# Kernel optimization log

Hardware: AMD Instinct MI355X
Metric: run time of the kernel (lower is better)

Reference implementation:

```python
import jax, jax.numpy as jnp
import numpy as np

HEADS = 16  # matches init_kwargs


def setup_inputs() -> dict:
    key = jax.random.key(0)
    ks = jax.random.split(key, 9)
    N, L, E, D = 2, 2048, 1024, 64
    return {
        "query": jax.random.normal(ks[0], (N, L, E), dtype=jnp.float32),
        "keys": jax.random.normal(ks[1], (N, L, E), dtype=jnp.float32),
        "values": jax.random.normal(ks[2], (N, L, E), dtype=jnp.float32),
        "masks": jax.random.randint(ks[3], (N, 1, 1, L), 0, 2, dtype=jnp.int32),
        "Wq": jax.random.normal(ks[4], (D, D), dtype=jnp.float32) / np.sqrt(D),
        "Wk": jax.random.normal(ks[5], (D, D), dtype=jnp.float32) / np.sqrt(D),
        "Wv": jax.random.normal(ks[6], (D, D), dtype=jnp.float32) / np.sqrt(D),
        "Wo": jax.random.normal(ks[7], (E, E), dtype=jnp.float32) / np.sqrt(E),
        "bo": jax.random.normal(ks[8], (E,), dtype=jnp.float32),
    }


def reference(query, keys, values, masks, Wq, Wk, Wv, Wo, bo):
    N, Lq, E = query.shape
    Lk = keys.shape[1]
    H = HEADS
    D = E // H
    # split heads: [N, L, H, D]
    q = query.reshape(N, Lq, H, D)
    k = keys.reshape(N, Lk, H, D)
    v = values.reshape(N, Lk, H, D)
    # per-head linear projections (weights shared across heads); Linear: x @ W.T
    q = jnp.einsum("nqhd,ed->nqhe", q, Wq)
    k = jnp.einsum("nkhd,ed->nkhe", k, Wk)
    v = jnp.einsum("nkhd,ed->nkhe", v, Wv)
    # scores [N, H, Lq, Lk]
    scores = jnp.einsum("nqhd,nkhd->nhqk", q, k)
    scores = jnp.where(masks == 0, jnp.float32(-1e20), scores)
    # NOTE: original scales by sqrt(embed_size), not sqrt(head_dim)
    attn = jax.nn.softmax(scores / jnp.sqrt(jnp.float32(E)), axis=3)
    out = jnp.einsum("nhqk,nkhd->nqhd", attn, v).reshape(N, Lq, E)
    return out @ Wo.T + bo
```

## Files before the change

kernel.cpp:

```cpp
#include <hip/hip_runtime.h>


typedef __bf16 bf16_t;
typedef __bf16 bf16x4 __attribute__((ext_vector_type(4)));
typedef __bf16 bf16x8 __attribute__((ext_vector_type(8)));
typedef float f32x4 __attribute__((ext_vector_type(4)));
typedef unsigned int u32x4 __attribute__((ext_vector_type(4)));

#define MFMA16(a, b, c) __builtin_amdgcn_mfma_f32_16x16x32_bf16((a), (b), (c), 0, 0, 0)

#define GLOAD_LDS16(gp, lp)                                              \
    __builtin_amdgcn_global_load_lds(                                    \
        (const __attribute__((address_space(1))) void*)(gp),             \
        (__attribute__((address_space(3))) void*)(lp), 16, 0, 0)

__device__ inline bf16x8 cvt8(const float* __restrict__ p) {
    f32x4 a = *(const f32x4*)p;
    f32x4 b = *(const f32x4*)(p + 4);
    bf16x8 r;
    r[0] = (bf16_t)a[0]; r[1] = (bf16_t)a[1];
    r[2] = (bf16_t)a[2]; r[3] = (bf16_t)a[3];
    r[4] = (bf16_t)b[0]; r[5] = (bf16_t)b[1];
    r[6] = (bf16_t)b[2]; r[7] = (bf16_t)b[3];
    return r;
}

__device__ inline bf16x8 cvt8s(const f32x4 a, const f32x4 b) {
    bf16x8 r;
    r[0] = (bf16_t)a[0]; r[1] = (bf16_t)a[1];
    r[2] = (bf16_t)a[2]; r[3] = (bf16_t)a[3];
    r[4] = (bf16_t)b[0]; r[5] = (bf16_t)b[1];
    r[6] = (bf16_t)b[2]; r[7] = (bf16_t)b[3];
    return r;
}

__device__ inline float exp2_fast(float x) {
    float r;
    asm("v_exp_f32 %0, %1" : "=v"(r) : "v"(x));
    return r;
}

__device__ inline unsigned cvt_pk_bf16(float lo, float hi) {
    unsigned r;
    asm("v_cvt_pk_bf16_f32 %0, %1, %2" : "=v"(r) : "v"(lo), "v"(hi));
    return r;
}

__device__ inline void xchg_quads(unsigned &x, unsigned &y) {
    asm("v_permlane32_swap_b32 %0, %1\n\t"
        "v_permlane16_swap_b32 %0, %1"
        : "+v"(x), "+v"(y));
}

__global__ __launch_bounds__(256) void scan_kernel(
    const int* __restrict__ msk, int* __restrict__ excl, int* __restrict__ lmap,
    const float* __restrict__ Wq, const float* __restrict__ Wk,
    const float* __restrict__ Wv,
    bf16_t* __restrict__ Wqb, bf16_t* __restrict__ Wkb, bf16_t* __restrict__ Wvb)
{
    const int t = threadIdx.x;

    if (blockIdx.x >= 2) {
        const int wi = blockIdx.x - 2;
        const float* Ws = (wi == 0) ? Wq : (wi == 1) ? Wk : Wv;
        bf16_t* Wb = (wi == 0) ? Wqb : (wi == 1) ? Wkb : Wvb;
        const float scale = (wi == 0) ? 0.04508422f : 1.0f;
        #pragma unroll
        for (int j = 0; j < 4; j++) {
            int idx = t * 16 + j * 4;
            f32x4 v = *(const f32x4*)&Ws[idx];
            bf16x4 r;
            r[0] = (bf16_t)(v[0] * scale); r[1] = (bf16_t)(v[1] * scale);
            r[2] = (bf16_t)(v[2] * scale); r[3] = (bf16_t)(v[3] * scale);
            *(bf16x4*)&Wb[idx] = r;
        }
        return;
    }

    __shared__ int wsum[4];
    const int n = blockIdx.x;
    const int lane = t & 63, w = t >> 6;
    const int* m = msk + n * 2048;
    int* e = excl + n * 2049;
    int* lm = lmap + n * 2048;

    int v[8], s = 0;
    #pragma unroll
    for (int j = 0; j < 8; j++) { v[j] = (m[t * 8 + j] != 0); s += v[j]; }

    int inc = s;
    #pragma unroll
    for (int d = 1; d < 64; d <<= 1) {
        int o = __shfl_up(inc, d);
        if (lane >= d) inc += o;
    }
    if (lane == 63) wsum[w] = inc;
    __syncthreads();
    int off = 0;
    #pragma unroll
    for (int i = 0; i < 4; i++)
        if (i < w) off += wsum[i];

    int a = off + inc - s;
    #pragma unroll
    for (int j = 0; j < 8; j++) {
        e[t * 8 + j] = a;
        if (v[j]) lm[a] = t * 8 + j;
        a += v[j];
    }
    if (t == 255) e[2048] = a;
}

__global__ __launch_bounds__(256) void qkv_proj_kernel(
    const float* __restrict__ kin, const float* __restrict__ vin,
    const bf16_t* __restrict__ Wkb, const bf16_t* __restrict__ Wvb,
    const float* __restrict__ Wo,
    const int* __restrict__ excl, const int* __restrict__ lmap,
    bf16_t* __restrict__ kc, bf16_t* __restrict__ vcT, bf16_t* __restrict__ Wob)
{
    __shared__ __align__(16) char smem[51200];

    const int t = threadIdx.x;
    const int w = t >> 6, lane = t & 63, quad = lane >> 4, l16 = lane & 15;

    if (blockIdx.y == 2) {
        int idx = blockIdx.x * 1024 + t * 4;
        f32x4 v = *(const f32x4*)&Wo[idx];
        bf16x4 r;
        r[0] = (bf16_t)v[0]; r[1] = (bf16_t)v[1];
        r[2] = (bf16_t)v[2]; r[3] = (bf16_t)v[3];
        *(bf16x4*)&Wob[idx] = r;
        return;
    }

    if (blockIdx.y == 1) {
        bf16_t* Ct = (bf16_t*)smem;
        const int h = blockIdx.x & 15;
        const int ctile = blockIdx.x >> 4;
        const int n = ctile >> 5;
        const int c0 = (ctile & 31) * 64;
        const int Lc = excl[n * 2049 + 2048];
        if (c0 >= Lc) return;

        const int p0 = w * 16 + l16;
        int cs = c0 + p0; if (cs > Lc - 1) cs = Lc - 1;
        const int tg = lmap[n * 2048 + cs];
        const size_t rb = ((size_t)(n * 2048 + tg)) * 1024 + h * 64;

        bf16x8 b0 = cvt8(&vin[rb + quad * 8]);
        bf16x8 b1 = cvt8(&vin[rb + 32 + quad * 8]);

        #pragma unroll
        for (int nt = 0; nt < 4; nt++) {
            bf16x8 a0 = *(const bf16x8*)&Wvb[(nt * 16 + l16) * 64 + quad * 8];
            bf16x8 a1 = *(const bf16x8*)&Wvb[(nt * 16 + l16) * 64 + 32 + quad * 8];
            f32x4 acc = {0.f, 0.f, 0.f, 0.f};
            acc = MFMA16(a0, b0, acc);
            acc = MFMA16(a1, b1, acc);
            #pragma unroll
            for (int r = 0; r < 4; r++)
                Ct[(nt * 16 + quad * 4 + r) * 72 + w * 16 + l16] = (bf16_t)acc[r];
        }
        __syncthreads();
        const int cnt = (Lc - c0 < 64) ? (Lc - c0) : 64;
        const size_t ob2 = ((size_t)(n * 16 + h)) * 131072 + c0;
        #pragma unroll
        for (int pass = 0; pass < 2; pass++) {
            int r = pass * 32 + (t >> 3);
            int cb8 = (t & 7) * 8;
            if (cb8 < cnt) {
                if (cb8 + 8 <= cnt) {
                    *(bf16x8*)&vcT[ob2 + (size_t)r * 2048 + cb8] =
                        *(const bf16x8*)&Ct[r * 72 + cb8];
                } else {
                    for (int q = cb8; q < cnt; q++)
                        vcT[ob2 + (size_t)r * 2048 + q] = Ct[r * 72 + q];
                }
            }
        }
        return;
    }

    if (blockIdx.x >= 512) return;
    const int n = blockIdx.x >> 8;
    const int c0 = (blockIdx.x & 255) * 8;
    const int Lc = excl[n * 2049 + 2048];
    if (c0 >= Lc) return;

    float* Xs = (float*)smem;
    bf16_t* Ct2 = (bf16_t*)(smem + 32768);

    #pragma unroll
    for (int j = 0; j < 8; j++) {
        int br = w * 32 + j * 4;
        int srow = br + (lane >> 4);
        int scol = ((lane & 15) ^ (srow & 15)) * 4;
        int csx = c0 + (srow >> 4); if (csx > Lc - 1) csx = Lc - 1;
        int hs = srow & 15;
        int ls = lmap[n * 2048 + csx];
        GLOAD_LDS16(&kin[((size_t)((n * 2048 + ls) * 16 + hs)) * 64 + scol], &Xs[br * 64]);
    }
    __syncthreads();

    const int rbase = w * 32;
    bf16x8 a[2][2];
    #pragma unroll
    for (int qs = 0; qs < 2; qs++) {
        int row = rbase + qs * 16 + l16;
        const char* rowp = (const char*)Xs + (size_t)row * 256;
        int swb = (row & 15) << 4;
        #pragma unroll
        for (int c = 0; c < 2; c++) {
            f32x4 lo = *(const f32x4*)(rowp + ((c * 128 + quad * 32) ^ swb));
            f32x4 hi = *(const f32x4*)(rowp + ((c * 128 + quad * 32 + 16) ^ swb));
            a[qs][c] = cvt8s(lo, hi);
        }
    }

    f32x4 acc[4][2];
    #pragma unroll
    for (int nt = 0; nt < 4; nt++) {
        bf16x8 b0 = *(const bf16x8*)&Wkb[(nt * 16 + l16) * 64 + quad * 8];
        bf16x8 b1 = *(const bf16x8*)&Wkb[(nt * 16 + l16) * 64 + 32 + quad * 8];
        #pragma unroll
        for (int qs = 0; qs < 2; qs++) {
            f32x4 z = {0.f, 0.f, 0.f, 0.f};
            z = MFMA16(a[qs][0], b0, z);
            z = MFMA16(a[qs][1], b1, z);
            acc[nt][qs] = z;
        }
    }

    #pragma unroll
    for (int nt = 0; nt < 4; nt++)
        #pragma unroll
        for (int qs = 0; qs < 2; qs++)
            #pragma unroll
            for (int r = 0; r < 4; r++)
                Ct2[(rbase + qs * 16 + quad * 4 + r) * 72 + nt * 16 + l16] = (bf16_t)acc[nt][qs][r];
    __syncthreads();

    #pragma unroll
    for (int it = 0; it < 4; it++) {
        int j = it * 32 + (t >> 3);
        bf16x8 val = *(const bf16x8*)&Ct2[j * 72 + (t & 7) * 8];
        int c = c0 + (j >> 4), h2 = j & 15;
        if (c < Lc)
            *(bf16x8*)&kc[(((size_t)(n * 16 + h2)) * 2048 + c) * 64 + (t & 7) * 8] = val;
    }
}

__global__ __launch_bounds__(256) void attn_kernel(
    const float* __restrict__ qin, const bf16_t* __restrict__ Wqb,
    const bf16_t* __restrict__ kc, const bf16_t* __restrict__ vcT,
    const int* __restrict__ excl, float* __restrict__ po, float* __restrict__ ls)
{
    __shared__ __align__(16) char smem[32768];
    bf16_t* KtP = (bf16_t*)smem;
    bf16_t* VtP = (bf16_t*)(smem + 16384);
#define KT(buf, r, c) KtP[(buf) * 4096 + (r) * 64 + (c)]
#define VT(buf, r, c) VtP[(buf) * 4096 + (r) * 64 + (c)]

    const int t = threadIdx.x;
    const int w = t >> 6, lane = t & 63, quad = lane >> 4, l16 = lane & 15;

    const int flat = blockIdx.x;
    const int xcd = flat & 7, slot = flat >> 3;
    const int nh = xcd * 4 + (slot >> 5);
    const int qb = (slot >> 1) & 15;
    const int s  = slot & 1;
    const int n = nh >> 4, h = nh & 15;
    const size_t nhbase = (size_t)nh * 131072;

    const int Lc = excl[n * 2049 + 2048];
    const int ntot  = (Lc + 63) >> 6;
    const int nhalf = (ntot + 1) >> 1;
    const int tile0 = s ? nhalf : 0;
    const int tile1 = s ? ntot : nhalf;
    const int rbase = w * 32;
    const int qbase = qb * 128 + rbase;

    bf16x8 aq[2][2];
    {
        float* Xq = (float*)smem;
        bf16_t* Qt = (bf16_t*)(smem + 16384);
        const int qrow0 = qb * 128;
        #pragma unroll
        for (int j = 0; j < 8; j++) {
            int br = w * 32 + j * 4;
            int srow = br + (lane >> 4);
            int scol = ((lane & 15) ^ (srow & 15)) * 4;
            GLOAD_LDS16(&qin[((size_t)(n * 2048 + qrow0 + srow)) * 1024 + h * 64 + scol],
                        &Xq[br * 64]);
        }
        __syncthreads();

        bf16x8 a[2][2];
        #pragma unroll
        for (int qs = 0; qs < 2; qs++) {
            int row = rbase + qs * 16 + l16;
            const char* rowp = (const char*)Xq + (size_t)row * 256;
            int swb = (row & 15) << 4;
            #pragma unroll
            for (int c = 0; c < 2; c++) {
                f32x4 lo = *(const f32x4*)(rowp + ((c * 128 + quad * 32) ^ swb));
                f32x4 hi = *(const f32x4*)(rowp + ((c * 128 + quad * 32 + 16) ^ swb));
                a[qs][c] = cvt8s(lo, hi);
            }
        }
        __syncthreads();

        f32x4 pacc[4][2];
        #pragma unroll
        for (int nt = 0; nt < 4; nt++) {
            bf16x8 b0 = *(const bf16x8*)&Wqb[(nt * 16 + l16) * 64 + quad * 8];
            bf16x8 b1 = *(const bf16x8*)&Wqb[(nt * 16 + l16) * 64 + 32 + quad * 8];
            #pragma unroll
            for (int qs = 0; qs < 2; qs++) {
                f32x4 z = {0.f, 0.f, 0.f, 0.f};
                z = MFMA16(a[qs][0], b0, z);
                z = MFMA16(a[qs][1], b1, z);
                pacc[nt][qs] = z;
            }
        }
        #pragma unroll
        for (int nt = 0; nt < 4; nt++)
            #pragma unroll
            for (int qs = 0; qs < 2; qs++)
                #pragma unroll
                for (int r = 0; r < 4; r++) {
                    int row = rbase + qs * 16 + quad * 4 + r;
                    int col = nt * 16 + l16;
                    int byteoff = row * 128 + ((((col >> 3) ^ (row & 7)) << 4) | ((col & 7) << 1));
                    *(bf16_t*)((char*)Qt + byteoff) = (bf16_t)pacc[nt][qs][r];
                }
        __syncthreads();
        #pragma unroll
        for (int qs = 0; qs < 2; qs++) {
            int row = rbase + qs * 16 + l16;
            #pragma unroll
            for (int c = 0; c < 2; c++)
                aq[qs][c] = *(const bf16x8*)((const char*)Qt + row * 128 +
                                             (((c * 4 + quad) ^ (row & 7)) << 4));
        }
        __syncthreads();
    }

    f32x4 o[2][4];
    float lsum[2] = {0.f, 0.f};
    #pragma unroll
    for (int qs = 0; qs < 2; qs++)
        #pragma unroll
        for (int dt = 0; dt < 4; dt++) {
            o[qs][dt][0] = 0.f; o[qs][dt][1] = 0.f; o[qs][dt][2] = 0.f; o[qs][dt][3] = 0.f;
        }

    const int ksrow = lane >> 3;
    const int kscol = ((lane & 7) ^ (lane >> 3)) * 8;
    const int swr = l16 & 7;
    const int ck0 = (quad ^ swr) * 8;
    const int ck1 = ((quad + 4) ^ swr) * 8;

#define STAGE_KV(buf, kn)                                                     \
    {                                                                         \
        _Pragma("unroll")                                                     \
        for (int j = 0; j < 2; j++) {                                         \
            int rb = w * 16 + j * 8;                                          \
            GLOAD_LDS16(&kc[nhbase + (size_t)((kn) + rb + ksrow) * 64 + kscol],\
                        &KT(buf, rb, 0));                                     \
            GLOAD_LDS16(&vcT[nhbase + (size_t)(rb + ksrow) * 2048 + (kn) + kscol],\
                        &VT(buf, rb, 0));                                     \
        }                                                                     \
    }

    if (tile0 < tile1) STAGE_KV(0, tile0 * 64);

    for (int i = tile0; i < tile1; i++) {
        const int cb = (i - tile0) & 1, nb = cb ^ 1;
        const int k0 = i * 64;
        __syncthreads();

        if (i + 1 < tile1) STAGE_KV(nb, k0 + 64);

        f32x4 st[2][4];
        __builtin_amdgcn_s_setprio(1);
        #pragma unroll
        for (int ct = 0; ct < 4; ct++) {
            bf16x8 kb0 = *(const bf16x8*)&KT(cb, ct * 16 + l16, ck0);
            bf16x8 kb1 = *(const bf16x8*)&KT(cb, ct * 16 + l16, ck1);
            #pragma unroll
            for (int qs = 0; qs < 2; qs++) {
                f32x4 acc = {0.f, 0.f, 0.f, 0.f};
                acc = MFMA16(kb0, aq[qs][0], acc);
                acc = MFMA16(kb1, aq[qs][1], acc);
                st[qs][ct] = acc;
            }
        }
        __builtin_amdgcn_s_setprio(0);

        if (k0 + 64 <= Lc) {
            #pragma unroll
            for (int qs = 0; qs < 2; qs++)
                #pragma unroll
                for (int ct = 0; ct < 4; ct++)
                    #pragma unroll
                    for (int r = 0; r < 4; r++) {
                        float p = exp2_fast(st[qs][ct][r]);
                        lsum[qs] += p;
                        st[qs][ct][r] = p;
                    }
        } else {
            #pragma unroll
            for (int qs = 0; qs < 2; qs++)
                #pragma unroll
                for (int ct = 0; ct < 4; ct++)
                    #pragma unroll
                    for (int r = 0; r < 4; r++) {
                        int kk = k0 + ct * 16 + quad * 4 + r;
                        float p = (kk < Lc) ? exp2_fast(st[qs][ct][r]) : 0.0f;
                        lsum[qs] += p;
                        st[qs][ct][r] = p;
                    }
        }

        bf16x8 bp[2][2];
        #pragma unroll
        for (int qs = 0; qs < 2; qs++) {
            unsigned u[4][2];
            #pragma unroll
            for (int ct = 0; ct < 4; ct++) {
                u[ct][0] = cvt_pk_bf16(st[qs][ct][0], st[qs][ct][1]);
                u[ct][1] = cvt_pk_bf16(st[qs][ct][2], st[qs][ct][3]);
            }
            #pragma unroll
            for (int hh = 0; hh < 2; hh++) {
                unsigned b0 = u[2 * hh][0], b2 = u[2 * hh + 1][0];
                xchg_quads(b0, b2);
                unsigned b1 = u[2 * hh][1], b3 = u[2 * hh + 1][1];
                xchg_quads(b1, b3);
                u32x4 q4 = {b0, b1, b2, b3};
                bp[qs][hh] = __builtin_bit_cast(bf16x8, q4);
            }
        }

        __builtin_amdgcn_s_setprio(1);
        #pragma unroll
        for (int dt = 0; dt < 4; dt++) {
            bf16x8 va0 = *(const bf16x8*)&VT(cb, dt * 16 + l16, ck0);
            bf16x8 va1 = *(const bf16x8*)&VT(cb, dt * 16 + l16, ck1);
            #pragma unroll
            for (int qs = 0; qs < 2; qs++) {
                o[qs][dt] = MFMA16(va0, bp[qs][0], o[qs][dt]);
                o[qs][dt] = MFMA16(va1, bp[qs][1], o[qs][dt]);
            }
        }
        __builtin_amdgcn_s_setprio(0);
    }

    #pragma unroll
    for (int qs = 0; qs < 2; qs++) {
        float v = lsum[qs];
        v += __shfl_xor(v, 16);
        v += __shfl_xor(v, 32);
        const int q = qbase + qs * 16 + l16;
        const size_t pbase = ((size_t)(nh * 2 + s) * 2048 + q) * 64;
        #pragma unroll
        for (int dt = 0; dt < 4; dt++)
            *(f32x4*)&po[pbase + dt * 16 + quad * 4] = o[qs][dt];
        if (lane < 16) ls[(size_t)(nh * 2 + s) * 2048 + q] = v;
    }
#undef KT
#undef VT
#undef STAGE_KV
}

__global__ __launch_bounds__(256) void combine_kernel(
    const float* __restrict__ po, const float* __restrict__ ls,
    bf16_t* __restrict__ ao)
{
    const int t = threadIdx.x;
    const int nh = blockIdx.x >> 6;
    const int qblk = blockIdx.x & 63;
    const int n = nh >> 4, h = nh & 15;
    const int q = qblk * 32 + (t >> 3);
    const int dc = (t & 7) * 8;

    float l0 = ls[(size_t)(nh * 2) * 2048 + q];
    float l1 = ls[(size_t)(nh * 2 + 1) * 2048 + q];
    float inv = 1.0f / (l0 + l1);

    size_t b0 = ((size_t)(nh * 2) * 2048 + q) * 64 + dc;
    size_t b1 = ((size_t)(nh * 2 + 1) * 2048 + q) * 64 + dc;
    f32x4 a0 = *(const f32x4*)&po[b0];
    f32x4 a1 = *(const f32x4*)&po[b0 + 4];
    f32x4 c0 = *(const f32x4*)&po[b1];
    f32x4 c1 = *(const f32x4*)&po[b1 + 4];

    bf16x8 r;
    r[0] = (bf16_t)((a0[0] + c0[0]) * inv);
    r[1] = (bf16_t)((a0[1] + c0[1]) * inv);
    r[2] = (bf16_t)((a0[2] + c0[2]) * inv);
    r[3] = (bf16_t)((a0[3] + c0[3]) * inv);
    r[4] = (bf16_t)((a1[0] + c1[0]) * inv);
    r[5] = (bf16_t)((a1[1] + c1[1]) * inv);
    r[6] = (bf16_t)((a1[2] + c1[2]) * inv);
    r[7] = (bf16_t)((a1[3] + c1[3]) * inv);
    *(bf16x8*)&ao[((size_t)n * 2048 + q) * 1024 + h * 64 + dc] = r;
}

__global__ __launch_bounds__(256, 2) void out_proj_kernel(
    const bf16_t* __restrict__ X, const bf16_t* __restrict__ Wob,
    const float* __restrict__ bo, float* __restrict__ out)
{
    __shared__ bf16_t Xs[2][128][64];
    __shared__ bf16_t Ws[2][64][64];

    const int t = threadIdx.x;
    const int w = t >> 6, lane = t & 63, quad = lane >> 4, l16 = lane & 15;
    const int Mbase = blockIdx.x * 128;
    const int Nbase = blockIdx.y * 64;
    const int mrow = (w & 1) * 64;
    const int ncol = (w >> 1) * 32;

    const int scol = ((lane & 7) ^ (lane >> 3)) * 8;
    const int swr  = l16 & 7;

    f32x4 acc[4][2];
    #pragma unroll
    for (int mi = 0; mi < 4; mi++)
        #pragma unroll
        for (int ni = 0; ni < 2; ni++) {
            acc[mi][ni][0] = 0.f; acc[mi][ni][1] = 0.f;
            acc[mi][ni][2] = 0.f; acc[mi][ni][3] = 0.f;
        }

    #pragma unroll
    for (int j = 0; j < 4; j++) {
        int br = w * 32 + j * 8;
        GLOAD_LDS16(&X[(size_t)(Mbase + br + (lane >> 3)) * 1024 + scol], &Xs[0][br][0]);
    }
    #pragma unroll
    for (int j = 0; j < 2; j++) {
        int br = w * 16 + j * 8;
        GLOAD_LDS16(&Wob[(size_t)(Nbase + br + (lane >> 3)) * 1024 + scol], &Ws[0][br][0]);
    }

    for (int i = 0; i < 16; i++) {
        const int cb = i & 1, nb = cb ^ 1;
        __syncthreads();

        if (i < 15) {
            const int kn = (i + 1) * 64;
            #pragma unroll
            for (int j = 0; j < 4; j++) {
                int br = w * 32 + j * 8;
                GLOAD_LDS16(&X[(size_t)(Mbase + br + (lane >> 3)) * 1024 + kn + scol],
                            &Xs[nb][br][0]);
            }
            #pragma unroll
            for (int j = 0; j < 2; j++) {
                int br = w * 16 + j * 8;
                GLOAD_LDS16(&Wob[(size_t)(Nbase + br + (lane >> 3)) * 1024 + kn + scol],
                            &Ws[nb][br][0]);
            }
        }

        #pragma unroll
        for (int c = 0; c < 2; c++) {
            bf16x8 bfr[2];
            #pragma unroll
            for (int ni = 0; ni < 2; ni++)
                bfr[ni] = *(const bf16x8*)&Ws[cb][ncol + ni * 16 + l16][((c * 4 + quad) ^ swr) * 8];
            #pragma unroll
            for (int mi = 0; mi < 4; mi++) {
                bf16x8 afr = *(const bf16x8*)&Xs[cb][mrow + mi * 16 + l16][((c * 4 + quad) ^ swr) * 8];
                #pragma unroll
                for (int ni = 0; ni < 2; ni++)
                    acc[mi][ni] = MFMA16(afr, bfr[ni], acc[mi][ni]);
            }
        }
    }

    #pragma unroll
    for (int ni = 0; ni < 2; ni++) {
        float b = bo[Nbase + ncol + ni * 16 + l16];
        #pragma unroll
        for (int mi = 0; mi < 4; mi++) {
            #pragma unroll
            for (int r = 0; r < 4; r++) {
                int row = Mbase + mrow + mi * 16 + quad * 4 + r;
                out[(size_t)row * 1024 + Nbase + ncol + ni * 16 + l16] = acc[mi][ni][r] + b;
            }
        }
    }
}

extern "C" void kernel_launch(void* const* d_in, const int* in_sizes, int n_in,
                              void* d_out, int out_size, void* d_ws, size_t ws_size,
                              hipStream_t stream)
{
    const float* qin = (const float*)d_in[0];
    const float* kin = (const float*)d_in[1];
    const float* vin = (const float*)d_in[2];
    const int*   msk = (const int*)d_in[3];
    const float* Wq  = (const float*)d_in[4];
    const float* Wk  = (const float*)d_in[5];
    const float* Wv  = (const float*)d_in[6];
    const float* Wo  = (const float*)d_in[7];
    const float* bo  = (const float*)d_in[8];
    float* out = (float*)d_out;

    bf16_t* ws  = (bf16_t*)d_ws;
    bf16_t* kc  = ws + 4194304;
    bf16_t* vcT = ws + 8388608;
    bf16_t* ao  = ws + 12582912;
    bf16_t* Wob = ws + 16777216;
    int* excl   = (int*)(ws + 17825792);
    int* lmap   = excl + 4100;
    bf16_t* Wqb = (bf16_t*)(lmap + 4096);
    bf16_t* Wkb = Wqb + 4096;
    bf16_t* Wvb = Wkb + 4096;
    float* po   = (float*)((char*)d_ws + (40u << 20));
    float* ls   = (float*)((char*)d_ws + (80u << 20));

    scan_kernel<<<5, 256, 0, stream>>>(msk, excl, lmap, Wq, Wk, Wv, Wqb, Wkb, Wvb);
    qkv_proj_kernel<<<dim3(1024, 3), 256, 0, stream>>>(kin, vin, Wkb, Wvb, Wo,
                                                        excl, lmap, kc, vcT, Wob);
    attn_kernel<<<dim3(1024), 256, 0, stream>>>(qin, Wqb, kc, vcT, excl, po, ls);
    combine_kernel<<<dim3(2048), 256, 0, stream>>>(po, ls, ao);
    out_proj_kernel<<<dim3(32, 16), 256, 0, stream>>>(ao, Wob, bo, out);
}
```

Baseline: 170.1 us.

## Drop split-K attention and combine kernel; compute row sums via MFMA with ones

The attention kernel no longer splits the key range across two blocks. Each of 512 blocks processes all key tiles and writes the normalized bf16 output directly, which removes the fp32 partial-output round trip and the separate combine kernel launch. Row sums of the probabilities are now built with an extra MFMA against a ones vector instead of scalar adds and cross-lane shuffles. The out_proj occupancy hint rises from 2 to 3 blocks per SM. In exchange the attention grid halves to 512 blocks, so on a GPU with many CUs occupancy and latency hiding may suffer, since each block now runs twice as long.

Measured after the change: 155.3 us. 1.09x faster.

```diff
diff --git a/kernel.cpp b/kernel.cpp
--- a/kernel.cpp
+++ b/kernel.cpp
@@ -253,7 +253,7 @@
 __global__ __launch_bounds__(256) void attn_kernel(
     const float* __restrict__ qin, const bf16_t* __restrict__ Wqb,
     const bf16_t* __restrict__ kc, const bf16_t* __restrict__ vcT,
-    const int* __restrict__ excl, float* __restrict__ po, float* __restrict__ ls)
+    const int* __restrict__ excl, bf16_t* __restrict__ ao)
 {
     __shared__ __align__(16) char smem[32768];
     bf16_t* KtP = (bf16_t*)smem;
@@ -266,17 +266,12 @@
 
     const int flat = blockIdx.x;
     const int xcd = flat & 7, slot = flat >> 3;
-    const int nh = xcd * 4 + (slot >> 5);
-    const int qb = (slot >> 1) & 15;
-    const int s  = slot & 1;
+    const int nh = xcd * 4 + (slot >> 4), qb = slot & 15;
     const int n = nh >> 4, h = nh & 15;
     const size_t nhbase = (size_t)nh * 131072;
 
     const int Lc = excl[n * 2049 + 2048];
-    const int ntot  = (Lc + 63) >> 6;
-    const int nhalf = (ntot + 1) >> 1;
-    const int tile0 = s ? nhalf : 0;
-    const int tile1 = s ? ntot : nhalf;
+    const int ntiles = (Lc + 63) >> 6;
     const int rbase = w * 32;
     const int qbase = qb * 128 + rbase;
 
@@ -346,14 +341,20 @@
         __syncthreads();
     }
 
+    bf16x8 ones;
+    #pragma unroll
+    for (int j = 0; j < 8; j++) ones[j] = (bf16_t)1.0f;
+
     f32x4 o[2][4];
-    float lsum[2] = {0.f, 0.f};
-    #pragma unroll
-    for (int qs = 0; qs < 2; qs++)
+    f32x4 acc_l[2];
+    #pragma unroll
+    for (int qs = 0; qs < 2; qs++) {
+        acc_l[qs][0] = 0.f; acc_l[qs][1] = 0.f; acc_l[qs][2] = 0.f; acc_l[qs][3] = 0.f;
         #pragma unroll
         for (int dt = 0; dt < 4; dt++) {
             o[qs][dt][0] = 0.f; o[qs][dt][1] = 0.f; o[qs][dt][2] = 0.f; o[qs][dt][3] = 0.f;
         }
+    }
 
     const int ksrow = lane >> 3;
     const int kscol = ((lane & 7) ^ (lane >> 3)) * 8;
@@ -373,14 +374,14 @@
         }                                                                     \
     }
 
-    if (tile0 < tile1) STAGE_KV(0, tile0 * 64);
-
-    for (int i = tile0; i < tile1; i++) {
-        const int cb = (i - tile0) & 1, nb = cb ^ 1;
+    STAGE_KV(0, 0);
+
+    for (int i = 0; i < ntiles; i++) {
+        const int cb = i & 1, nb = cb ^ 1;
         const int k0 = i * 64;
         __syncthreads();
 
-        if (i + 1 < tile1) STAGE_KV(nb, k0 + 64);
+        if (i + 1 < ntiles) STAGE_KV(nb, k0 + 64);
 
         f32x4 st[2][4];
         __builtin_amdgcn_s_setprio(1);
@@ -404,11 +405,8 @@
                 #pragma unroll
                 for (int ct = 0; ct < 4; ct++)
                     #pragma unroll
-                    for (int r = 0; r < 4; r++) {
-                        float p = exp2_fast(st[qs][ct][r]);
-                        lsum[qs] += p;
-                        st[qs][ct][r] = p;
-                    }
+                    for (int r = 0; r < 4; r++)
+                        st[qs][ct][r] = exp2_fast(st[qs][ct][r]);
         } else {
             #pragma unroll
             for (int qs = 0; qs < 2; qs++)
@@ -417,9 +415,7 @@
                     #pragma unroll
                     for (int r = 0; r < 4; r++) {
                         int kk = k0 + ct * 16 + quad * 4 + r;
-                        float p = (kk < Lc) ? exp2_fast(st[qs][ct][r]) : 0.0f;
-                        lsum[qs] += p;
-                        st[qs][ct][r] = p;
+                        st[qs][ct][r] = (kk < Lc) ? exp2_fast(st[qs][ct][r]) : 0.0f;
                     }
         }
 
@@ -445,6 +441,11 @@
 
         __builtin_amdgcn_s_setprio(1);
         #pragma unroll
+        for (int qs = 0; qs < 2; qs++) {
+            acc_l[qs] = MFMA16(ones, bp[qs][0], acc_l[qs]);
+            acc_l[qs] = MFMA16(ones, bp[qs][1], acc_l[qs]);
+        }
+        #pragma unroll
         for (int dt = 0; dt < 4; dt++) {
             bf16x8 va0 = *(const bf16x8*)&VT(cb, dt * 16 + l16, ck0);
             bf16x8 va1 = *(const bf16x8*)&VT(cb, dt * 16 + l16, ck1);
@@ -459,56 +460,23 @@
 
     #pragma unroll
     for (int qs = 0; qs < 2; qs++) {
-        float v = lsum[qs];
-        v += __shfl_xor(v, 16);
-        v += __shfl_xor(v, 32);
+        float inv = 1.0f / acc_l[qs][0];
         const int q = qbase + qs * 16 + l16;
-        const size_t pbase = ((size_t)(nh * 2 + s) * 2048 + q) * 64;
-        #pragma unroll
-        for (int dt = 0; dt < 4; dt++)
-            *(f32x4*)&po[pbase + dt * 16 + quad * 4] = o[qs][dt];
-        if (lane < 16) ls[(size_t)(nh * 2 + s) * 2048 + q] = v;
+        const size_t base = ((size_t)n * 2048 + q) * 1024 + h * 64;
+        #pragma unroll
+        for (int dt = 0; dt < 4; dt++) {
+            bf16x4 ov;
+            #pragma unroll
+            for (int r = 0; r < 4; r++) ov[r] = (bf16_t)(o[qs][dt][r] * inv);
+            *(bf16x4*)&ao[base + dt * 16 + quad * 4] = ov;
+        }
     }
 #undef KT
 #undef VT
 #undef STAGE_KV
 }
 
-__global__ __launch_bounds__(256) void combine_kernel(
-    const float* __restrict__ po, const float* __restrict__ ls,
-    bf16_t* __restrict__ ao)
-{
-    const int t = threadIdx.x;
-    const int nh = blockIdx.x >> 6;
-    const int qblk = blockIdx.x & 63;
-    const int n = nh >> 4, h = nh & 15;
-    const int q = qblk * 32 + (t >> 3);
-    const int dc = (t & 7) * 8;
-
-    float l0 = ls[(size_t)(nh * 2) * 2048 + q];
-    float l1 = ls[(size_t)(nh * 2 + 1) * 2048 + q];
-    float inv = 1.0f / (l0 + l1);
-
-    size_t b0 = ((size_t)(nh * 2) * 2048 + q) * 64 + dc;
-    size_t b1 = ((size_t)(nh * 2 + 1) * 2048 + q) * 64 + dc;
-    f32x4 a0 = *(const f32x4*)&po[b0];
-    f32x4 a1 = *(const f32x4*)&po[b0 + 4];
-    f32x4 c0 = *(const f32x4*)&po[b1];
-    f32x4 c1 = *(const f32x4*)&po[b1 + 4];
-
-    bf16x8 r;
-    r[0] = (bf16_t)((a0[0] + c0[0]) * inv);
-    r[1] = (bf16_t)((a0[1] + c0[1]) * inv);
-    r[2] = (bf16_t)((a0[2] + c0[2]) * inv);
-    r[3] = (bf16_t)((a0[3] + c0[3]) * inv);
-    r[4] = (bf16_t)((a1[0] + c1[0]) * inv);
-    r[5] = (bf16_t)((a1[1] + c1[1]) * inv);
-    r[6] = (bf16_t)((a1[2] + c1[2]) * inv);
-    r[7] = (bf16_t)((a1[3] + c1[3]) * inv);
-    *(bf16x8*)&ao[((size_t)n * 2048 + q) * 1024 + h * 64 + dc] = r;
-}
-
-__global__ __launch_bounds__(256, 2) void out_proj_kernel(
+__global__ __launch_bounds__(256, 3) void out_proj_kernel(
     const bf16_t* __restrict__ X, const bf16_t* __restrict__ Wob,
     const float* __restrict__ bo, float* __restrict__ out)
 {
@@ -620,13 +588,10 @@
     bf16_t* Wqb = (bf16_t*)(lmap + 4096);
     bf16_t* Wkb = Wqb + 4096;
     bf16_t* Wvb = Wkb + 4096;
-    float* po   = (float*)((char*)d_ws + (40u << 20));
-    float* ls   = (float*)((char*)d_ws + (80u << 20));
 
     scan_kernel<<<5, 256, 0, stream>>>(msk, excl, lmap, Wq, Wk, Wv, Wqb, Wkb, Wvb);
     qkv_proj_kernel<<<dim3(1024, 3), 256, 0, stream>>>(kin, vin, Wkb, Wvb, Wo,
                                                         excl, lmap, kc, vcT, Wob);
-    attn_kernel<<<dim3(1024), 256, 0, stream>>>(qin, Wqb, kc, vcT, excl, po, ls);
-    combine_kernel<<<dim3(2048), 256, 0, stream>>>(po, ls, ao);
+    attn_kernel<<<dim3(512), 256, 0, stream>>>(qin, Wqb, kc, vcT, excl, ao);
     out_proj_kernel<<<dim3(32, 16), 256, 0, stream>>>(ao, Wob, bo, out);
 }
```
